# Optimization experiments

Hardware: AMD Instinct MI355X
Metric: run time of the kernel (lower is better)

Reference implementation:

```python
import jax, jax.numpy as jnp
import numpy as np

def setup_inputs() -> dict:
    key = jax.random.key(0)
    k1, k2, k3, k4 = jax.random.split(key, 4)
    B, T, C, D = 4, 4096, 1024, 128
    x = jax.random.normal(k1, (B, T, C), dtype=jnp.float32)
    Wq = jax.random.normal(k2, (C, D), dtype=jnp.float32) * (C ** -0.5)
    Wk = jax.random.normal(k3, (C, D), dtype=jnp.float32) * (C ** -0.5)
    Wv = jax.random.normal(k4, (C, D), dtype=jnp.float32) * (C ** -0.5)
    return {"x": x, "Wq": Wq, "Wk": Wk, "Wv": Wv}

def reference(x, Wq, Wk, Wv):
    # x: [B,T,C]; Wq/Wk/Wv: [C,D] (nn.Linear bias=False => x @ W)
    B, T, C = x.shape
    q = jnp.einsum('btc,cd->btd', x, Wq)  # [B,T,D]
    k = jnp.einsum('btc,cd->btd', x, Wk)
    v = jnp.einsum('btc,cd->btd', x, Wv)
    dk = q.shape[-1]
    scale = dk ** -0.5
    w = jnp.einsum('btd,bsd->bts', q, k) * scale  # [B,T,T]
    causal = jnp.tril(jnp.ones((T, T), dtype=bool))
    w = jnp.where(causal, w, -jnp.inf)
    w = jax.nn.softmax(w, axis=-1)
    # dropout p=0.0 => identity
    attention = jnp.einsum('bts,bsd->btd', w, v)  # [B,T,D]
    return attention
```

## Files before the change

### kernel.cpp

```cpp
#include <hip/hip_runtime.h>
#include <stdint.h>

typedef __bf16 bf16_t;
typedef bf16_t bf16x8 __attribute__((ext_vector_type(8)));
typedef float f32x4 __attribute__((ext_vector_type(4)));
typedef unsigned short us8 __attribute__((ext_vector_type(8)));
typedef unsigned short us4 __attribute__((ext_vector_type(4)));
typedef unsigned int u32x4 __attribute__((ext_vector_type(4)));

#define B_ 4
#define T_ 4096
#define C_ 1024
#define D_ 128

#define NCHUNK_PB 288
#define QSCALE 0.12751744f
#define M0 14.0f

__device__ __forceinline__ uint16_t f2bf(float f) {
    union { float f; uint32_t u; } v; v.f = f;
    uint32_t u = v.u;
    uint32_t r = (u + 0x7fffu + ((u >> 16) & 1u)) >> 16;
    return (uint16_t)r;
}

__device__ __forceinline__ uint16_t bfru(float f) {
    return (uint16_t)((__float_as_uint(f) + 0x8000u) >> 16);
}

__device__ __forceinline__ float bf2f(uint16_t u) {
    return __uint_as_float((uint32_t)u << 16);
}

__device__ __forceinline__ void gload_lds16(const void* g, void* l) {
    __builtin_amdgcn_global_load_lds(
        (const __attribute__((address_space(1))) void*)g,
        (__attribute__((address_space(3))) void*)l, 16, 0, 0);
}

__global__ __launch_bounds__(256) void prep_w(const float* __restrict__ Wq,
                                              const float* __restrict__ Wk,
                                              const float* __restrict__ Wv,
                                              uint16_t* __restrict__ WT) {
    int idx = blockIdx.x * 256 + threadIdx.x;
    if (idx >= 3 * D_ * C_) return;
    int w   = idx / (D_ * C_);
    int rem = idx - w * (D_ * C_);
    int n   = rem / C_;
    int k   = rem - n * C_;
    const float* W = (w == 0) ? Wq : (w == 1) ? Wk : Wv;
    WT[idx] = f2bf(W[(size_t)k * D_ + n]);
}

#define GST 72

__global__ __launch_bounds__(256) void qkv_gemm(const float* __restrict__ x,
                                                const uint16_t* __restrict__ WT,
                                                uint16_t* __restrict__ qb,
                                                uint16_t* __restrict__ kb,
                                                uint16_t* __restrict__ vT) {
    __shared__ __align__(16) uint16_t A_lds[64 * GST];
    __shared__ __align__(16) uint16_t W_lds[128 * GST];

    int tid  = threadIdx.x;
    int lane = tid & 63;
    int wave = tid >> 6;
    int quad = lane >> 4;
    int lx   = lane & 15;
    int wm   = wave >> 1, wn = wave & 1;

    int bx   = blockIdx.x;
    int wsel = bx % 3;
    int m0   = (bx / 3) * 64;
    const uint16_t* Wp = WT + (size_t)wsel * (D_ * C_);

    f32x4 acc[2][4];
    for (int mf = 0; mf < 2; mf++)
        for (int nf = 0; nf < 4; nf++)
            acc[mf][nf] = (f32x4){0.f, 0.f, 0.f, 0.f};

    int arow = tid >> 2, acb = (tid & 3) * 16;
    int wrow = tid >> 1, wcb = (tid & 1) * 32;

    for (int k0 = 0; k0 < C_; k0 += 64) {
        {
            const float* xp = x + (size_t)(m0 + arow) * C_ + k0 + acb;
            uint32_t d[8];
#pragma unroll
            for (int j = 0; j < 4; j++) {
                float4 f = *(const float4*)(xp + j * 4);
                uint32_t u0 = __float_as_uint(f.x) + 0x8000u;
                uint32_t u1 = __float_as_uint(f.y) + 0x8000u;
                uint32_t u2 = __float_as_uint(f.z) + 0x8000u;
                uint32_t u3 = __float_as_uint(f.w) + 0x8000u;
                d[2 * j]     = __builtin_amdgcn_perm(u1, u0, 0x07060302);
                d[2 * j + 1] = __builtin_amdgcn_perm(u3, u2, 0x07060302);
            }
            *(u32x4*)&A_lds[arow * GST + acb]     = (u32x4){d[0], d[1], d[2], d[3]};
            *(u32x4*)&A_lds[arow * GST + acb + 8] = (u32x4){d[4], d[5], d[6], d[7]};
        }
        {
            const uint16_t* wp = Wp + (size_t)wrow * C_ + k0 + wcb;
#pragma unroll
            for (int i = 0; i < 4; i++)
                *(us8*)&W_lds[wrow * GST + wcb + i * 8] = *(const us8*)(wp + i * 8);
        }
        __syncthreads();

#pragma unroll
        for (int kc = 0; kc < 2; kc++) {
            bf16x8 af[2];
#pragma unroll
            for (int mf = 0; mf < 2; mf++)
                af[mf] = *(const bf16x8*)&A_lds[(wm * 32 + mf * 16 + lx) * GST + kc * 32 + quad * 8];
#pragma unroll
            for (int nf = 0; nf < 4; nf++) {
                bf16x8 bf = *(const bf16x8*)&W_lds[(wn * 64 + nf * 16 + lx) * GST + kc * 32 + quad * 8];
                acc[0][nf] = __builtin_amdgcn_mfma_f32_16x16x32_bf16(af[0], bf, acc[0][nf], 0, 0, 0);
                acc[1][nf] = __builtin_amdgcn_mfma_f32_16x16x32_bf16(af[1], bf, acc[1][nf], 0, 0, 0);
            }
        }
        __syncthreads();
    }

    int mrow0 = m0 + wm * 32 + quad * 4;
    if (wsel == 2) {
#pragma unroll
        for (int mf = 0; mf < 2; mf++) {
            int mbase = mrow0 + mf * 16;
            int batch = mbase >> 12;
            int t     = mbase & 4095;
#pragma unroll
            for (int nf = 0; nf < 4; nf++) {
                int n = wn * 64 + nf * 16 + lx;
                us4 pv;
#pragma unroll
                for (int r = 0; r < 4; r++) pv[r] = bfru(acc[mf][nf][r]);
                *(us4*)&vT[(size_t)batch * D_ * T_ + (size_t)n * T_ + t] = pv;
            }
        }
    } else {
        uint16_t* dst = (wsel == 0) ? qb : kb;
        float sc = (wsel == 0) ? QSCALE : 1.0f;
#pragma unroll
        for (int mf = 0; mf < 2; mf++)
#pragma unroll
            for (int nf = 0; nf < 4; nf++) {
                int n = wn * 64 + nf * 16 + lx;
#pragma unroll
                for (int r = 0; r < 4; r++)
                    dst[(size_t)(mrow0 + mf * 16 + r) * D_ + n] = bfru(acc[mf][nf][r] * sc);
            }
    }
}

__global__ __launch_bounds__(256, 2) void attn(const uint16_t* __restrict__ qb,
                                               const uint16_t* __restrict__ kb,
                                               const uint16_t* __restrict__ vT,
                                               uint16_t* __restrict__ part,
                                               float* __restrict__ ml) {
    __shared__ __align__(16) uint16_t K_lds[2][64 * 128];
    __shared__ __align__(16) uint16_t V_lds[2][128 * 64];
    __shared__ __align__(16) uint16_t P_lds[4 * 16 * 64];

    int tid  = threadIdx.x;
    int lane = tid & 63;
    int wave = tid >> 6;
    int quad = lane >> 4;
    int lx   = lane & 15;
    int lx7  = lx & 7;

    int batch = blockIdx.x & 3;
    int L     = NCHUNK_PB - 1 - (blockIdx.x >> 2);
    int g = 0;
    while (g < 7 && 4 * (g + 1) * (g + 2) <= L) g++;
    int rem   = L - 4 * g * (g + 1);
    int jt    = 8 * g + rem / (g + 1);
    int chunk = rem - (rem / (g + 1)) * (g + 1);
    int lidx  = batch * NCHUNK_PB + L;

    int q0     = jt * 64;
    int st0    = chunk * 8;
    int ntiles = min(8, jt - st0 + 1);

    auto issue_kv = [&](int bi, int tile) {
        int s0i = tile * 64;
        const uint16_t* kB = kb + (size_t)(batch * T_ + s0i) * D_;
#pragma unroll
        for (int j = 0; j < 4; j++) {
            int row = wave * 16 + j * 4 + (lane >> 4);
            int gch = (lane & 15) ^ (row & 7);
            gload_lds16(kB + (size_t)row * D_ + gch * 8,
                        &K_lds[bi][(wave * 16 + j * 4) * 128]);
        }
        const uint16_t* vB = vT + (size_t)batch * D_ * T_ + s0i;
#pragma unroll
        for (int j = 0; j < 4; j++) {
            int row = wave * 32 + j * 8 + (lane >> 3);
            int gch = (lane & 7) ^ (row & 7);
            gload_lds16(vB + (size_t)row * T_ + gch * 8,
                        &V_lds[bi][(wave * 32 + j * 8) * 64]);
        }
    };

    bf16x8 qf[4];
    {
        const uint16_t* qp = qb + (size_t)(batch * T_ + q0 + wave * 16 + lx) * D_ + quad * 8;
#pragma unroll
        for (int kc = 0; kc < 4; kc++) qf[kc] = *(const bf16x8*)(qp + kc * 32);
    }

    f32x4 o[8];
    for (int i = 0; i < 8; i++) o[i] = (f32x4){0.f, 0.f, 0.f, 0.f};
    float l_i[4] = {0.f, 0.f, 0.f, 0.f};

    issue_kv(0, st0);
    int cur = 0;

    for (int it = 0; it < ntiles; it++) {
        int s0 = (st0 + it) * 64;
        __syncthreads();
        if (it + 1 < ntiles) issue_kv(cur ^ 1, st0 + it + 1);

        f32x4 s[4];
        for (int nf = 0; nf < 4; nf++) s[nf] = (f32x4){0.f, 0.f, 0.f, 0.f};
        __builtin_amdgcn_s_setprio(1);
#pragma unroll
        for (int kc = 0; kc < 4; kc++)
#pragma unroll
            for (int nf = 0; nf < 4; nf++) {
                bf16x8 kf = *(const bf16x8*)&K_lds[cur][(nf * 16 + lx) * 128 + (((kc * 4 + quad) ^ lx7) * 8)];
                s[nf] = __builtin_amdgcn_mfma_f32_16x16x32_bf16(qf[kc], kf, s[nf], 0, 0, 0);
            }
        __builtin_amdgcn_s_setprio(0);

        float p[4][4];
#pragma unroll
        for (int nf = 0; nf < 4; nf++)
#pragma unroll
            for (int r = 0; r < 4; r++) p[nf][r] = s[nf][r];

        if (st0 + it == jt) {
            int rowg = q0 + wave * 16 + quad * 4;
#pragma unroll
            for (int nf = 0; nf < 4; nf++) {
                int colg = s0 + nf * 16 + lx;
#pragma unroll
                for (int r = 0; r < 4; r++)
                    if (colg > rowg + r) p[nf][r] = -INFINITY;
            }
        }

#pragma unroll
        for (int nf = 0; nf < 4; nf++)
#pragma unroll
            for (int r = 0; r < 4; r++)
                p[nf][r] = exp2f(p[nf][r] - M0);
#pragma unroll
        for (int r = 0; r < 4; r++)
            l_i[r] += (p[0][r] + p[1][r]) + (p[2][r] + p[3][r]);

#pragma unroll
        for (int nf = 0; nf < 4; nf++)
#pragma unroll
            for (int r = 0; r < 4; r++) {
                uint32_t u  = __float_as_uint(p[nf][r]) + 0x8000u;
                uint32_t pu = (uint32_t)__shfl_xor((int)u, 1, 64);
                uint32_t pk = __builtin_amdgcn_perm(pu, u, 0x07060302);
                if ((lane & 1) == 0) {
                    int prow = quad * 4 + r;
                    int pchk = nf * 2 + (lx >> 3);
                    *(uint32_t*)&P_lds[wave * 1024 + prow * 64 + ((pchk ^ (prow & 7)) * 8) + lx7] = pk;
                }
            }

        bf16x8 pf[2];
        pf[0] = *(const bf16x8*)&P_lds[wave * 1024 + lx * 64 + ((quad ^ lx7) * 8)];
        pf[1] = *(const bf16x8*)&P_lds[wave * 1024 + lx * 64 + (((4 + quad) ^ lx7) * 8)];
        __builtin_amdgcn_s_setprio(1);
#pragma unroll
        for (int nf = 0; nf < 8; nf++)
#pragma unroll
            for (int kc = 0; kc < 2; kc++) {
                bf16x8 vf = *(const bf16x8*)&V_lds[cur][(nf * 16 + lx) * 64 + (((kc * 4 + quad) ^ lx7) * 8)];
                o[nf] = __builtin_amdgcn_mfma_f32_16x16x32_bf16(pf[kc], vf, o[nf], 0, 0, 0);
            }
        __builtin_amdgcn_s_setprio(0);
        cur ^= 1;
    }

#pragma unroll
    for (int off = 1; off < 16; off <<= 1)
#pragma unroll
        for (int r = 0; r < 4; r++)
            l_i[r] += __shfl_xor(l_i[r], off, 64);

    uint16_t* pp = part + (size_t)lidx * (64 * 128);
#pragma unroll
    for (int nf = 0; nf < 8; nf++)
#pragma unroll
        for (int r = 0; r < 4; r++) {
            int lrow = wave * 16 + quad * 4 + r;
            pp[lrow * 128 + nf * 16 + lx] = bfru(o[nf][r]);
        }
    if (lx == 0) {
#pragma unroll
        for (int r = 0; r < 4; r++)
            ml[(size_t)lidx * 64 + wave * 16 + quad * 4 + r] = l_i[r];
    }
}

__global__ __launch_bounds__(256) void combine(const uint16_t* __restrict__ part,
                                               const float* __restrict__ ml,
                                               float* __restrict__ out) {
    int bidx  = blockIdx.x;
    int half  = bidx & 1;
    int jt    = (bidx >> 1) & 63;
    int batch = bidx >> 7;
    int g     = jt >> 3;
    int base  = batch * NCHUNK_PB + jt + g * (jt - 4 * g - 4);
    int nch   = g + 1;

    int tid  = threadIdx.x;
    int lrow = tid >> 2;
    int c0   = half * 64 + (tid & 3) * 16;

    float Lsum = 0.f;
    f32x4 acc[4];
#pragma unroll
    for (int i = 0; i < 4; i++) acc[i] = (f32x4){0.f, 0.f, 0.f, 0.f};

    for (int c = 0; c < nch; c++) {
        Lsum += ml[(size_t)(base + c) * 64 + lrow];
        const uint16_t* p = part + (size_t)(base + c) * (64 * 128) + lrow * 128 + c0;
#pragma unroll
        for (int i = 0; i < 2; i++) {
            us8 v = *(const us8*)(p + i * 8);
#pragma unroll
            for (int j = 0; j < 8; j++)
                acc[i * 2 + (j >> 2)][j & 3] += bf2f(v[j]);
        }
    }
    float inv = 1.f / Lsum;
    size_t row = (size_t)(batch * T_ + jt * 64 + lrow);
#pragma unroll
    for (int i = 0; i < 4; i++)
        *(f32x4*)(out + row * 128 + c0 + i * 4) = acc[i] * inv;
}

extern "C" void kernel_launch(void* const* d_in, const int* in_sizes, int n_in,
                              void* d_out, int out_size, void* d_ws, size_t ws_size,
                              hipStream_t stream) {
    const float* x  = (const float*)d_in[0];
    const float* Wq = (const float*)d_in[1];
    const float* Wk = (const float*)d_in[2];
    const float* Wv = (const float*)d_in[3];
    float* out = (float*)d_out;

    uint16_t* ws = (uint16_t*)d_ws;
    uint16_t* qb = ws;
    uint16_t* kb = qb + (size_t)16384 * 128;
    uint16_t* vT = kb + (size_t)16384 * 128;
    uint16_t* WT = vT + (size_t)16384 * 128;
    uint16_t* part = WT + (size_t)3 * D_ * C_;
    float* ml = (float*)(part + (size_t)4 * NCHUNK_PB * 64 * 128);

    prep_w<<<dim3((3 * D_ * C_ + 255) / 256), dim3(256), 0, stream>>>(Wq, Wk, Wv, WT);
    qkv_gemm<<<dim3(3 * (16384 / 64)), dim3(256), 0, stream>>>(x, WT, qb, kb, vT);
    attn<<<dim3(B_ * NCHUNK_PB), dim3(256), 0, stream>>>(qb, kb, vT, part, ml);
    combine<<<dim3(B_ * (T_ / 64) * 2), dim3(256), 0, stream>>>(part, ml, out);
}
```

Before: 197.0 us.

## Double attention query tile to 128 rows per block for K/V reuse

Measured after the change: 205.5 us. 1.04x slower.

```diff
diff --git a/kernel.cpp b/kernel.cpp
--- a/kernel.cpp
+++ b/kernel.cpp
@@ -13,7 +13,7 @@
 #define C_ 1024
 #define D_ 128
 
-#define NCHUNK_PB 288
+#define NCHUNK_PB 144
 #define QSCALE 0.12751744f
 #define M0 14.0f
 
@@ -161,7 +161,7 @@
                                                float* __restrict__ ml) {
     __shared__ __align__(16) uint16_t K_lds[2][64 * 128];
     __shared__ __align__(16) uint16_t V_lds[2][128 * 64];
-    __shared__ __align__(16) uint16_t P_lds[4 * 16 * 64];
+    __shared__ __align__(16) uint16_t P_lds[4 * 32 * 64];
 
     int tid  = threadIdx.x;
     int lane = tid & 63;
@@ -172,16 +172,16 @@
 
     int batch = blockIdx.x & 3;
     int L     = NCHUNK_PB - 1 - (blockIdx.x >> 2);
-    int g = 0;
-    while (g < 7 && 4 * (g + 1) * (g + 2) <= L) g++;
-    int rem   = L - 4 * g * (g + 1);
-    int jt    = 8 * g + rem / (g + 1);
-    int chunk = rem - (rem / (g + 1)) * (g + 1);
+    int a = 0;
+    while (a < 7 && 2 * (a + 1) * (a + 2) <= L) a++;
+    int rem   = L - 2 * a * (a + 1);
+    int jt    = 4 * a + rem / (a + 1);
+    int chunk = rem - (rem / (a + 1)) * (a + 1);
     int lidx  = batch * NCHUNK_PB + L;
 
-    int q0     = jt * 64;
+    int q0     = jt * 128;
     int st0    = chunk * 8;
-    int ntiles = min(8, jt - st0 + 1);
+    int ntiles = min(8, 2 * jt + 2 - st0);
 
     auto issue_kv = [&](int bi, int tile) {
         int s0i = tile * 64;
@@ -203,16 +203,20 @@
         }
     };
 
-    bf16x8 qf[4];
-    {
-        const uint16_t* qp = qb + (size_t)(batch * T_ + q0 + wave * 16 + lx) * D_ + quad * 8;
-#pragma unroll
-        for (int kc = 0; kc < 4; kc++) qf[kc] = *(const bf16x8*)(qp + kc * 32);
-    }
-
-    f32x4 o[8];
-    for (int i = 0; i < 8; i++) o[i] = (f32x4){0.f, 0.f, 0.f, 0.f};
-    float l_i[4] = {0.f, 0.f, 0.f, 0.f};
+    bf16x8 qf[2][4];
+#pragma unroll
+    for (int mf = 0; mf < 2; mf++) {
+        const uint16_t* qp = qb + (size_t)(batch * T_ + q0 + wave * 32 + mf * 16 + lx) * D_ + quad * 8;
+#pragma unroll
+        for (int kc = 0; kc < 4; kc++) qf[mf][kc] = *(const bf16x8*)(qp + kc * 32);
+    }
+
+    f32x4 o[2][8];
+#pragma unroll
+    for (int mf = 0; mf < 2; mf++)
+#pragma unroll
+        for (int i = 0; i < 8; i++) o[mf][i] = (f32x4){0.f, 0.f, 0.f, 0.f};
+    float l_i[2][4] = {{0.f, 0.f, 0.f, 0.f}, {0.f, 0.f, 0.f, 0.f}};
 
     issue_kv(0, st0);
     int cur = 0;
@@ -222,68 +226,86 @@
         __syncthreads();
         if (it + 1 < ntiles) issue_kv(cur ^ 1, st0 + it + 1);
 
-        f32x4 s[4];
-        for (int nf = 0; nf < 4; nf++) s[nf] = (f32x4){0.f, 0.f, 0.f, 0.f};
+        f32x4 s[2][4];
+#pragma unroll
+        for (int mf = 0; mf < 2; mf++)
+#pragma unroll
+            for (int nf = 0; nf < 4; nf++) s[mf][nf] = (f32x4){0.f, 0.f, 0.f, 0.f};
         __builtin_amdgcn_s_setprio(1);
 #pragma unroll
         for (int kc = 0; kc < 4; kc++)
 #pragma unroll
             for (int nf = 0; nf < 4; nf++) {
                 bf16x8 kf = *(const bf16x8*)&K_lds[cur][(nf * 16 + lx) * 128 + (((kc * 4 + quad) ^ lx7) * 8)];
-                s[nf] = __builtin_amdgcn_mfma_f32_16x16x32_bf16(qf[kc], kf, s[nf], 0, 0, 0);
+                s[0][nf] = __builtin_amdgcn_mfma_f32_16x16x32_bf16(qf[0][kc], kf, s[0][nf], 0, 0, 0);
+                s[1][nf] = __builtin_amdgcn_mfma_f32_16x16x32_bf16(qf[1][kc], kf, s[1][nf], 0, 0, 0);
             }
         __builtin_amdgcn_s_setprio(0);
 
-        float p[4][4];
-#pragma unroll
-        for (int nf = 0; nf < 4; nf++)
-#pragma unroll
-            for (int r = 0; r < 4; r++) p[nf][r] = s[nf][r];
-
-        if (st0 + it == jt) {
-            int rowg = q0 + wave * 16 + quad * 4;
-#pragma unroll
-            for (int nf = 0; nf < 4; nf++) {
-                int colg = s0 + nf * 16 + lx;
+        float p[2][4][4];
+#pragma unroll
+        for (int mf = 0; mf < 2; mf++)
+#pragma unroll
+            for (int nf = 0; nf < 4; nf++)
+#pragma unroll
+                for (int r = 0; r < 4; r++) p[mf][nf][r] = s[mf][nf][r];
+
+        if (st0 + it >= 2 * jt) {
+#pragma unroll
+            for (int mf = 0; mf < 2; mf++) {
+                int rowg = q0 + wave * 32 + mf * 16 + quad * 4;
+#pragma unroll
+                for (int nf = 0; nf < 4; nf++) {
+                    int colg = s0 + nf * 16 + lx;
+#pragma unroll
+                    for (int r = 0; r < 4; r++)
+                        if (colg > rowg + r) p[mf][nf][r] = -INFINITY;
+                }
+            }
+        }
+
+#pragma unroll
+        for (int mf = 0; mf < 2; mf++) {
+#pragma unroll
+            for (int nf = 0; nf < 4; nf++)
 #pragma unroll
                 for (int r = 0; r < 4; r++)
-                    if (colg > rowg + r) p[nf][r] = -INFINITY;
-            }
-        }
-
-#pragma unroll
-        for (int nf = 0; nf < 4; nf++)
+                    p[mf][nf][r] = exp2f(p[mf][nf][r] - M0);
 #pragma unroll
             for (int r = 0; r < 4; r++)
-                p[nf][r] = exp2f(p[nf][r] - M0);
-#pragma unroll
-        for (int r = 0; r < 4; r++)
-            l_i[r] += (p[0][r] + p[1][r]) + (p[2][r] + p[3][r]);
-
-#pragma unroll
-        for (int nf = 0; nf < 4; nf++)
-#pragma unroll
-            for (int r = 0; r < 4; r++) {
-                uint32_t u  = __float_as_uint(p[nf][r]) + 0x8000u;
-                uint32_t pu = (uint32_t)__shfl_xor((int)u, 1, 64);
-                uint32_t pk = __builtin_amdgcn_perm(pu, u, 0x07060302);
-                if ((lane & 1) == 0) {
-                    int prow = quad * 4 + r;
-                    int pchk = nf * 2 + (lx >> 3);
-                    *(uint32_t*)&P_lds[wave * 1024 + prow * 64 + ((pchk ^ (prow & 7)) * 8) + lx7] = pk;
+                l_i[mf][r] += (p[mf][0][r] + p[mf][1][r]) + (p[mf][2][r] + p[mf][3][r]);
+        }
+
+#pragma unroll
+        for (int mf = 0; mf < 2; mf++)
+#pragma unroll
+            for (int nf = 0; nf < 4; nf++)
+#pragma unroll
+                for (int r = 0; r < 4; r++) {
+                    uint32_t u  = __float_as_uint(p[mf][nf][r]) + 0x8000u;
+                    uint32_t pu = (uint32_t)__shfl_xor((int)u, 1, 64);
+                    uint32_t pk = __builtin_amdgcn_perm(pu, u, 0x07060302);
+                    if ((lane & 1) == 0) {
+                        int prow = mf * 16 + quad * 4 + r;
+                        int pchk = nf * 2 + (lx >> 3);
+                        *(uint32_t*)&P_lds[wave * 2048 + prow * 64 + ((pchk ^ (prow & 7)) * 8) + lx7] = pk;
+                    }
                 }
-            }
-
-        bf16x8 pf[2];
-        pf[0] = *(const bf16x8*)&P_lds[wave * 1024 + lx * 64 + ((quad ^ lx7) * 8)];
-        pf[1] = *(const bf16x8*)&P_lds[wave * 1024 + lx * 64 + (((4 + quad) ^ lx7) * 8)];
+
+        bf16x8 pf[2][2];
+#pragma unroll
+        for (int mf = 0; mf < 2; mf++) {
+            pf[mf][0] = *(const bf16x8*)&P_lds[wave * 2048 + (mf * 16 + lx) * 64 + ((quad ^ lx7) * 8)];
+            pf[mf][1] = *(const bf16x8*)&P_lds[wave * 2048 + (mf * 16 + lx) * 64 + (((4 + quad) ^ lx7) * 8)];
+        }
         __builtin_amdgcn_s_setprio(1);
 #pragma unroll
         for (int nf = 0; nf < 8; nf++)
 #pragma unroll
             for (int kc = 0; kc < 2; kc++) {
                 bf16x8 vf = *(const bf16x8*)&V_lds[cur][(nf * 16 + lx) * 64 + (((kc * 4 + quad) ^ lx7) * 8)];
-                o[nf] = __builtin_amdgcn_mfma_f32_16x16x32_bf16(pf[kc], vf, o[nf], 0, 0, 0);
+                o[0][nf] = __builtin_amdgcn_mfma_f32_16x16x32_bf16(pf[0][kc], vf, o[0][nf], 0, 0, 0);
+                o[1][nf] = __builtin_amdgcn_mfma_f32_16x16x32_bf16(pf[1][kc], vf, o[1][nf], 0, 0, 0);
             }
         __builtin_amdgcn_s_setprio(0);
         cur ^= 1;
@@ -292,21 +314,27 @@
 #pragma unroll
     for (int off = 1; off < 16; off <<= 1)
 #pragma unroll
-        for (int r = 0; r < 4; r++)
-            l_i[r] += __shfl_xor(l_i[r], off, 64);
-
-    uint16_t* pp = part + (size_t)lidx * (64 * 128);
-#pragma unroll
-    for (int nf = 0; nf < 8; nf++)
-#pragma unroll
-        for (int r = 0; r < 4; r++) {
-            int lrow = wave * 16 + quad * 4 + r;
-            pp[lrow * 128 + nf * 16 + lx] = bfru(o[nf][r]);
-        }
+        for (int mf = 0; mf < 2; mf++)
+#pragma unroll
+            for (int r = 0; r < 4; r++)
+                l_i[mf][r] += __shfl_xor(l_i[mf][r], off, 64);
+
+    uint16_t* pp = part + (size_t)lidx * (128 * 128);
+#pragma unroll
+    for (int mf = 0; mf < 2; mf++)
+#pragma unroll
+        for (int nf = 0; nf < 8; nf++)
+#pragma unroll
+            for (int r = 0; r < 4; r++) {
+                int lrow = wave * 32 + mf * 16 + quad * 4 + r;
+                pp[lrow * 128 + nf * 16 + lx] = bfru(o[mf][nf][r]);
+            }
     if (lx == 0) {
 #pragma unroll
-        for (int r = 0; r < 4; r++)
-            ml[(size_t)lidx * 64 + wave * 16 + quad * 4 + r] = l_i[r];
+        for (int mf = 0; mf < 2; mf++)
+#pragma unroll
+            for (int r = 0; r < 4; r++)
+                ml[(size_t)lidx * 128 + wave * 32 + mf * 16 + quad * 4 + r] = l_i[mf][r];
     }
 }
 
@@ -315,26 +343,26 @@
                                                float* __restrict__ out) {
     int bidx  = blockIdx.x;
     int half  = bidx & 1;
-    int jt    = (bidx >> 1) & 63;
-    int batch = bidx >> 7;
-    int g     = jt >> 3;
-    int base  = batch * NCHUNK_PB + jt + g * (jt - 4 * g - 4);
-    int nch   = g + 1;
+    int jt    = (bidx >> 1) & 31;
+    int batch = bidx >> 6;
+    int a     = jt >> 2;
+    int base  = batch * NCHUNK_PB + 2 * a * (a + 1) + (jt - 4 * a) * (a + 1);
+    int nch   = a + 1;
 
     int tid  = threadIdx.x;
-    int lrow = tid >> 2;
-    int c0   = half * 64 + (tid & 3) * 16;
+    int lrow = tid >> 1;
+    int c0   = half * 64 + (tid & 1) * 32;
 
     float Lsum = 0.f;
-    f32x4 acc[4];
-#pragma unroll
-    for (int i = 0; i < 4; i++) acc[i] = (f32x4){0.f, 0.f, 0.f, 0.f};
+    f32x4 acc[8];
+#pragma unroll
+    for (int i = 0; i < 8; i++) acc[i] = (f32x4){0.f, 0.f, 0.f, 0.f};
 
     for (int c = 0; c < nch; c++) {
-        Lsum += ml[(size_t)(base + c) * 64 + lrow];
-        const uint16_t* p = part + (size_t)(base + c) * (64 * 128) + lrow * 128 + c0;
-#pragma unroll
-        for (int i = 0; i < 2; i++) {
+        Lsum += ml[(size_t)(base + c) * 128 + lrow];
+        const uint16_t* p = part + (size_t)(base + c) * (128 * 128) + lrow * 128 + c0;
+#pragma unroll
+        for (int i = 0; i < 4; i++) {
             us8 v = *(const us8*)(p + i * 8);
 #pragma unroll
             for (int j = 0; j < 8; j++)
@@ -342,9 +370,9 @@
         }
     }
     float inv = 1.f / Lsum;
-    size_t row = (size_t)(batch * T_ + jt * 64 + lrow);
-#pragma unroll
-    for (int i = 0; i < 4; i++)
+    size_t row = (size_t)(batch * T_ + jt * 128 + lrow);
+#pragma unroll
+    for (int i = 0; i < 8; i++)
         *(f32x4*)(out + row * 128 + c0 + i * 4) = acc[i] * inv;
 }
 
@@ -363,10 +391,10 @@
     uint16_t* vT = kb + (size_t)16384 * 128;
     uint16_t* WT = vT + (size_t)16384 * 128;
     uint16_t* part = WT + (size_t)3 * D_ * C_;
-    float* ml = (float*)(part + (size_t)4 * NCHUNK_PB * 64 * 128);
+    float* ml = (float*)(part + (size_t)4 * NCHUNK_PB * 128 * 128);
 
     prep_w<<<dim3((3 * D_ * C_ + 255) / 256), dim3(256), 0, stream>>>(Wq, Wk, Wv, WT);
     qkv_gemm<<<dim3(3 * (16384 / 64)), dim3(256), 0, stream>>>(x, WT, qb, kb, vT);
     attn<<<dim3(B_ * NCHUNK_PB), dim3(256), 0, stream>>>(qb, kb, vT, part, ml);
-    combine<<<dim3(B_ * (T_ / 64) * 2), dim3(256), 0, stream>>>(part, ml, out);
-}
+    combine<<<dim3(B_ * 32 * 2), dim3(256), 0, stream>>>(part, ml, out);
+}
```
